# Performance work log

Measured on AMD Instinct MI355X. Metric: run time of the kernel, lower is better.

Reference implementation:

```python
import jax, jax.numpy as jnp
import numpy as np

N = 8192
IN_DIM = 256
HID = 512
NUM_CLASSES = 256
AVG_DEG = 32


def setup_inputs() -> dict:
    key = jax.random.key(0)
    k_a, k_x, k_w1, k_w2 = jax.random.split(key, 4)
    # Binary adjacency with avg degree ~AVG_DEG (entries are exactly 1.0, matching
    # A.nonzero() edge extraction with implicit unit edge weights).
    A = (jax.random.uniform(k_a, (N, N)) < (AVG_DEG / N)).astype(jnp.float32)
    x = jax.random.normal(k_x, (N, IN_DIM), dtype=jnp.float32)
    # GCNConv params: glorot-ish weights, zero bias.
    W1 = jax.random.normal(k_w1, (IN_DIM, HID), dtype=jnp.float32) / np.sqrt(IN_DIM)
    b1 = jnp.zeros((HID,), dtype=jnp.float32)
    W2 = jax.random.normal(k_w2, (HID, NUM_CLASSES), dtype=jnp.float32) / np.sqrt(HID)
    b2 = jnp.zeros((NUM_CLASSES,), dtype=jnp.float32)
    sigmoid_param = jnp.array([10.0], dtype=jnp.float32)
    return {"A": A, "x": x, "W1": W1, "b1": b1, "W2": W2, "b2": b2,
            "sigmoid_param": sigmoid_param}


def _gcn_propagate(A, deg_inv_sqrt, h):
    # PyG GCNConv aggregation with self-loops, without materializing A + I:
    # out_j = d_j^{-1/2} * sum_i A_ij d_i^{-1/2} h_i  +  d_j^{-1} h_j
    m = deg_inv_sqrt[:, None] * h              # [N, d]
    agg = A.T @ m                              # messages flow row -> col
    return deg_inv_sqrt[:, None] * agg + (deg_inv_sqrt[:, None] ** 2) * h


def reference(A, x, W1, b1, W2, b2, sigmoid_param):
    # Degree from column sums of (A + I) — matches gcn_norm's scatter on col.
    deg = jnp.sum(A, axis=0) + 1.0             # [N], >= 1 thanks to self-loop
    deg_inv_sqrt = jax.lax.rsqrt(deg)
    skip_x = x                                  # nn.Identity skip connection
    # GCNConv 1: linear then normalized aggregation, then bias; ReLU.
    h = _gcn_propagate(A, deg_inv_sqrt, x @ W1) + b1
    h = jax.nn.relu(h)
    # GCNConv 2.
    h = _gcn_propagate(A, deg_inv_sqrt, h @ W2) + b2
    # Skip add + scaled sigmoid (original casts to double; kept float32 here).
    return jax.nn.sigmoid(sigmoid_param * (h + skip_x))
```

## Files before the change

kernel.cpp:

```cpp
#include <hip/hip_runtime.h>
#include <hip/hip_bf16.h>

#define N_NODES 8192
#define IN_DIM  256
#define HID     512
#define NCLS    256
#define CAP     128

typedef __attribute__((ext_vector_type(8))) __bf16 bf16x8;
typedef __attribute__((ext_vector_type(4))) float  floatx4;

static __device__ __forceinline__ float bf2f(ushort u) {
    union { float f; unsigned int i; } v; v.i = ((unsigned int)u) << 16; return v.f;
}
static __device__ __forceinline__ ushort f2bf(float f) {
    __hip_bfloat16 b = __float2bfloat16(f);
    return *reinterpret_cast<ushort*>(&b);
}
static __device__ __forceinline__ void bfpair(unsigned int u, float& lo, float& hi) {
    union { float f; unsigned int i; } a, b;
    a.i = u << 16; b.i = u & 0xFFFF0000u;
    lo = a.f; hi = b.f;
}

__global__ __launch_bounds__(256) void build_csc(const float* __restrict__ A,
                                                 int* __restrict__ col_cnt,
                                                 int* __restrict__ col_idx) {
    const int jbase = (blockIdx.x * 256 + threadIdx.x) * 4;
    const int i0 = blockIdx.y * 32;
    for (int ii = 0; ii < 32; ++ii) {
        const int i = i0 + ii;
        const floatx4* p = reinterpret_cast<const floatx4*>(A + (size_t)i * N_NODES + jbase);
        floatx4 v = __builtin_nontemporal_load(p);
        if (v.x != 0.0f) { int q = atomicAdd(&col_cnt[jbase + 0], 1); if (q < CAP) col_idx[(size_t)(jbase + 0) * CAP + q] = i; }
        if (v.y != 0.0f) { int q = atomicAdd(&col_cnt[jbase + 1], 1); if (q < CAP) col_idx[(size_t)(jbase + 1) * CAP + q] = i; }
        if (v.z != 0.0f) { int q = atomicAdd(&col_cnt[jbase + 2], 1); if (q < CAP) col_idx[(size_t)(jbase + 2) * CAP + q] = i; }
        if (v.w != 0.0f) { int q = atomicAdd(&col_cnt[jbase + 3], 1); if (q < CAP) col_idx[(size_t)(jbase + 3) * CAP + q] = i; }
    }
}

__global__ __launch_bounds__(256) void prep_misc(const float* __restrict__ x,
                                                 const float* __restrict__ W1,
                                                 const float* __restrict__ W2,
                                                 const int* __restrict__ col_cnt,
                                                 ushort* __restrict__ xb,
                                                 float* __restrict__ dis,
                                                 ushort* __restrict__ W1Th, ushort* __restrict__ W1Tl,
                                                 ushort* __restrict__ W2Th, ushort* __restrict__ W2Tl) {
    const int idx = blockIdx.x * 256 + threadIdx.x;
    {
        const int i = idx * 4;
        const floatx4 v = *reinterpret_cast<const floatx4*>(x + i);
        *reinterpret_cast<ushort4*>(xb + i) = ushort4{f2bf(v.x), f2bf(v.y), f2bf(v.z), f2bf(v.w)};
    }
    if (idx < N_NODES)
        dis[idx] = rsqrtf((float)col_cnt[idx] + 1.0f);
    if (idx < IN_DIM * HID) {
        {
            const int k = idx / HID, n = idx % HID;
            const float v = W1[idx]; const ushort h = f2bf(v);
            W1Th[(size_t)n * IN_DIM + k] = h;
            W1Tl[(size_t)n * IN_DIM + k] = f2bf(v - bf2f(h));
        }
        {
            const int k = idx / NCLS, n = idx % NCLS;
            const float v = W2[idx]; const ushort h = f2bf(v);
            W2Th[(size_t)n * HID + k] = h;
            W2Tl[(size_t)n * HID + k] = f2bf(v - bf2f(h));
        }
    }
}

__global__ __launch_bounds__(256) void agg_x(const ushort* __restrict__ xb,
                                             const int* __restrict__ col_idx,
                                             const int* __restrict__ col_cnt,
                                             const float* __restrict__ dis,
                                             ushort* __restrict__ px) {
    const int j = __builtin_amdgcn_readfirstlane(blockIdx.x * 4 + (threadIdx.x >> 6));
    const int d = (threadIdx.x & 63) * 4;
    const int cnt = min(col_cnt[j], CAP);
    const float dj = dis[j];
    float a0, a1, a2, a3;
    {
        const uint2 sv = *reinterpret_cast<const uint2*>(xb + (size_t)j * IN_DIM + d);
        float f0, f1, f2, f3;
        bfpair(sv.x, f0, f1); bfpair(sv.y, f2, f3);
        a0 = dj * f0; a1 = dj * f1; a2 = dj * f2; a3 = dj * f3;
    }
    const int* __restrict__ lst = col_idx + (size_t)j * CAP;
    int e = 0;
    for (; e + 8 <= cnt; e += 8) {
        uint2 rv[8]; float we[8];
#pragma unroll
        for (int q = 0; q < 8; ++q) {
            const int i = lst[e + q];
            rv[q] = *reinterpret_cast<const uint2*>(xb + (size_t)i * IN_DIM + d);
            we[q] = dis[i];
        }
#pragma unroll
        for (int q = 0; q < 8; ++q) {
            float f0, f1, f2, f3;
            bfpair(rv[q].x, f0, f1); bfpair(rv[q].y, f2, f3);
            a0 += we[q] * f0; a1 += we[q] * f1; a2 += we[q] * f2; a3 += we[q] * f3;
        }
    }
    for (; e < cnt; ++e) {
        const int i = lst[e];
        const uint2 rv = *reinterpret_cast<const uint2*>(xb + (size_t)i * IN_DIM + d);
        const float we = dis[i];
        float f0, f1, f2, f3;
        bfpair(rv.x, f0, f1); bfpair(rv.y, f2, f3);
        a0 += we * f0; a1 += we * f1; a2 += we * f2; a3 += we * f3;
    }
    a0 *= dj; a1 *= dj; a2 *= dj; a3 *= dj;
    *reinterpret_cast<ushort4*>(px + (size_t)j * IN_DIM + d) =
        ushort4{f2bf(a0), f2bf(a1), f2bf(a2), f2bf(a3)};
}

template<int K>
__device__ __forceinline__ void gemm_core44(const ushort* __restrict__ A,
                                            const ushort* __restrict__ Bh,
                                            const ushort* __restrict__ Bl,
                                            int m_base, int n_base,
                                            int l16, int quad, floatx4 acc[4][4]) {
#pragma unroll 2
    for (int k0 = 0; k0 < K; k0 += 32) {
        const int kf = k0 + quad * 8;
        bf16x8 a[4], bh[4], bl[4];
#pragma unroll
        for (int t = 0; t < 4; ++t)
            a[t] = *reinterpret_cast<const bf16x8*>(A + (size_t)(m_base + t * 16 + l16) * K + kf);
#pragma unroll
        for (int t = 0; t < 4; ++t) {
            const size_t bo = (size_t)(n_base + t * 16 + l16) * K + kf;
            bh[t] = *reinterpret_cast<const bf16x8*>(Bh + bo);
            bl[t] = *reinterpret_cast<const bf16x8*>(Bl + bo);
        }
#pragma unroll
        for (int tm = 0; tm < 4; ++tm)
#pragma unroll
            for (int tn = 0; tn < 4; ++tn) {
                acc[tm][tn] = __builtin_amdgcn_mfma_f32_16x16x32_bf16(a[tm], bl[tn], acc[tm][tn], 0, 0, 0);
                acc[tm][tn] = __builtin_amdgcn_mfma_f32_16x16x32_bf16(a[tm], bh[tn], acc[tm][tn], 0, 0, 0);
            }
    }
}

template<int K>
__device__ __forceinline__ void gemm_core42(const ushort* __restrict__ A,
                                            const ushort* __restrict__ Bh,
                                            const ushort* __restrict__ Bl,
                                            int m_base, int n_base,
                                            int l16, int quad, floatx4 acc[4][2]) {
#pragma unroll 2
    for (int k0 = 0; k0 < K; k0 += 32) {
        const int kf = k0 + quad * 8;
        bf16x8 a[4], bh[2], bl[2];
#pragma unroll
        for (int t = 0; t < 4; ++t)
            a[t] = *reinterpret_cast<const bf16x8*>(A + (size_t)(m_base + t * 16 + l16) * K + kf);
#pragma unroll
        for (int t = 0; t < 2; ++t) {
            const size_t bo = (size_t)(n_base + t * 16 + l16) * K + kf;
            bh[t] = *reinterpret_cast<const bf16x8*>(Bh + bo);
            bl[t] = *reinterpret_cast<const bf16x8*>(Bl + bo);
        }
#pragma unroll
        for (int tm = 0; tm < 4; ++tm)
#pragma unroll
            for (int tn = 0; tn < 2; ++tn) {
                acc[tm][tn] = __builtin_amdgcn_mfma_f32_16x16x32_bf16(a[tm], bl[tn], acc[tm][tn], 0, 0, 0);
                acc[tm][tn] = __builtin_amdgcn_mfma_f32_16x16x32_bf16(a[tm], bh[tn], acc[tm][tn], 0, 0, 0);
            }
    }
}

__global__ __launch_bounds__(256) void gemm1_fused(const ushort* __restrict__ A,
                                                   const ushort* __restrict__ Bh,
                                                   const ushort* __restrict__ Bl,
                                                   const float* __restrict__ b1,
                                                   ushort* __restrict__ h) {
    const int tid = threadIdx.x;
    const int lane = tid & 63, wave = tid >> 6;
    const int wm = wave >> 1, wn = wave & 1;
    const int l16 = lane & 15, quad = lane >> 4;
    const int m_base = blockIdx.x * 128 + wm * 64;
    const int n_base = blockIdx.y * 128 + wn * 64;
    floatx4 acc[4][4] = {};
    gemm_core44<IN_DIM>(A, Bh, Bl, m_base, n_base, l16, quad, acc);
#pragma unroll
    for (int tn = 0; tn < 4; ++tn) {
        const int col = n_base + tn * 16 + l16;
        const float bv = b1[col];
#pragma unroll
        for (int tm = 0; tm < 4; ++tm)
#pragma unroll
            for (int r = 0; r < 4; ++r) {
                const int row = m_base + tm * 16 + quad * 4 + r;
                h[(size_t)row * HID + col] = f2bf(fmaxf(acc[tm][tn][r] + bv, 0.0f));
            }
    }
}

__global__ __launch_bounds__(256) void gemm2(const ushort* __restrict__ A,
                                             const ushort* __restrict__ Bh,
                                             const ushort* __restrict__ Bl,
                                             ushort* __restrict__ g2b) {
    const int tid = threadIdx.x;
    const int lane = tid & 63, wave = tid >> 6;
    const int wm = wave >> 1, wn = wave & 1;
    const int l16 = lane & 15, quad = lane >> 4;
    const int m_base = blockIdx.x * 128 + wm * 64;
    const int n_base = blockIdx.y * 64 + wn * 32;
    floatx4 acc[4][2] = {};
    gemm_core42<HID>(A, Bh, Bl, m_base, n_base, l16, quad, acc);
#pragma unroll
    for (int tm = 0; tm < 4; ++tm)
#pragma unroll
        for (int tn = 0; tn < 2; ++tn)
#pragma unroll
            for (int r = 0; r < 4; ++r)
                g2b[(size_t)(m_base + tm * 16 + quad * 4 + r) * NCLS + (n_base + tn * 16 + l16)] =
                    f2bf(acc[tm][tn][r]);
}

__global__ __launch_bounds__(256) void agg_out(const ushort* __restrict__ g2b,
                                               const int* __restrict__ col_idx,
                                               const int* __restrict__ col_cnt,
                                               const float* __restrict__ dis,
                                               const float* __restrict__ b2,
                                               const float* __restrict__ x,
                                               const float* __restrict__ sp_p,
                                               float* __restrict__ out) {
    const int j = __builtin_amdgcn_readfirstlane(blockIdx.x * 4 + (threadIdx.x >> 6));
    const int d = (threadIdx.x & 63) * 4;
    const int cnt = min(col_cnt[j], CAP);
    const float dj = dis[j];
    float a0, a1, a2, a3;
    {
        const uint2 sv = *reinterpret_cast<const uint2*>(g2b + (size_t)j * NCLS + d);
        float f0, f1, f2, f3;
        bfpair(sv.x, f0, f1); bfpair(sv.y, f2, f3);
        a0 = dj * f0; a1 = dj * f1; a2 = dj * f2; a3 = dj * f3;
    }
    const int* __restrict__ lst = col_idx + (size_t)j * CAP;
    int e = 0;
    for (; e + 8 <= cnt; e += 8) {
        uint2 rv[8]; float we[8];
#pragma unroll
        for (int q = 0; q < 8; ++q) {
            const int i = lst[e + q];
            rv[q] = *reinterpret_cast<const uint2*>(g2b + (size_t)i * NCLS + d);
            we[q] = dis[i];
        }
#pragma unroll
        for (int q = 0; q < 8; ++q) {
            float f0, f1, f2, f3;
            bfpair(rv[q].x, f0, f1); bfpair(rv[q].y, f2, f3);
            a0 += we[q] * f0; a1 += we[q] * f1; a2 += we[q] * f2; a3 += we[q] * f3;
        }
    }
    for (; e < cnt; ++e) {
        const int i = lst[e];
        const uint2 rv = *reinterpret_cast<const uint2*>(g2b + (size_t)i * NCLS + d);
        const float we = dis[i];
        float f0, f1, f2, f3;
        bfpair(rv.x, f0, f1); bfpair(rv.y, f2, f3);
        a0 += we * f0; a1 += we * f1; a2 += we * f2; a3 += we * f3;
    }
    const float sp = sp_p[0];
    const floatx4 bv = *reinterpret_cast<const floatx4*>(b2 + d);
    const floatx4 xv = __builtin_nontemporal_load(
        reinterpret_cast<const floatx4*>(x + (size_t)j * NCLS + d));
    floatx4 o;
    o.x = 1.0f / (1.0f + __expf(-sp * (dj * a0 + bv.x + xv.x)));
    o.y = 1.0f / (1.0f + __expf(-sp * (dj * a1 + bv.y + xv.y)));
    o.z = 1.0f / (1.0f + __expf(-sp * (dj * a2 + bv.z + xv.z)));
    o.w = 1.0f / (1.0f + __expf(-sp * (dj * a3 + bv.w + xv.w)));
    __builtin_nontemporal_store(o, reinterpret_cast<floatx4*>(out + (size_t)j * NCLS + d));
}

extern "C" void kernel_launch(void* const* d_in, const int* in_sizes, int n_in,
                              void* d_out, int out_size, void* d_ws, size_t ws_size,
                              hipStream_t stream) {
    const float* A  = (const float*)d_in[0];
    const float* x  = (const float*)d_in[1];
    const float* W1 = (const float*)d_in[2];
    const float* b1 = (const float*)d_in[3];
    const float* W2 = (const float*)d_in[4];
    const float* b2 = (const float*)d_in[5];
    const float* sp = (const float*)d_in[6];
    float* out = (float*)d_out;

    char* ws = (char*)d_ws;
    size_t off = 0;
    auto alloc = [&](size_t bytes) {
        void* p = ws + off;
        off = (off + bytes + 255) & ~(size_t)255;
        return p;
    };
    int*    col_cnt = (int*)   alloc((size_t)N_NODES * 4);
    float*  dis     = (float*) alloc((size_t)N_NODES * 4);
    int*    col_idx = (int*)   alloc((size_t)N_NODES * CAP * 4);
    ushort* xb      = (ushort*)alloc((size_t)N_NODES * IN_DIM * 2);
    ushort* px      = (ushort*)alloc((size_t)N_NODES * IN_DIM * 2);
    ushort* W1Th    = (ushort*)alloc((size_t)HID * IN_DIM * 2);
    ushort* W1Tl    = (ushort*)alloc((size_t)HID * IN_DIM * 2);
    ushort* W2Th    = (ushort*)alloc((size_t)NCLS * HID * 2);
    ushort* W2Tl    = (ushort*)alloc((size_t)NCLS * HID * 2);
    ushort* h       = (ushort*)alloc((size_t)N_NODES * HID * 2);
    ushort* g2b     = (ushort*)alloc((size_t)N_NODES * NCLS * 2);

    (void)hipMemsetAsync(col_cnt, 0, (size_t)N_NODES * 4, stream);

    build_csc<<<dim3(8, 256), 256, 0, stream>>>(A, col_cnt, col_idx);
    prep_misc<<<(N_NODES * IN_DIM / 4) / 256, 256, 0, stream>>>(
        x, W1, W2, col_cnt, xb, dis, W1Th, W1Tl, W2Th, W2Tl);

    agg_x<<<N_NODES / 4, 256, 0, stream>>>(xb, col_idx, col_cnt, dis, px);
    gemm1_fused<<<dim3(N_NODES / 128, HID / 128), 256, 0, stream>>>(
        px, W1Th, W1Tl, b1, h);

    gemm2<<<dim3(N_NODES / 128, NCLS / 64), 256, 0, stream>>>(
        h, W2Th, W2Tl, g2b);
    agg_out<<<N_NODES / 4, 256, 0, stream>>>(g2b, col_idx, col_cnt, dis, b2, x, sp, out);
}
```

Baseline: 427.8 us.

## Fuse both GEMMs into one kernel keeping hidden activations in LDS

Merges the first GEMM (with bias and ReLU) and the second GEMM into a single kernel. Each block computes a 32-row slab of the hidden layer across all 512 columns into shared memory, then multiplies it by W2 directly from LDS. This removes the global write and re-read of the 8192x512 hidden tensor and one kernel launch. In exchange, each block now reloads the full W1 and W2 hi/lo weights for only 32 rows, and there are fewer, larger blocks holding 16 accumulator tiles per wave, which raises register pressure and may lower occupancy.

```diff
diff --git a/kernel.cpp b/kernel.cpp
--- a/kernel.cpp
+++ b/kernel.cpp
@@ -6,6 +6,7 @@
 #define HID     512
 #define NCLS    256
 #define CAP     128
+#define LDSK    (HID + 8)
 
 typedef __attribute__((ext_vector_type(8))) __bf16 bf16x8;
 typedef __attribute__((ext_vector_type(4))) float  floatx4;
@@ -117,111 +118,91 @@
         ushort4{f2bf(a0), f2bf(a1), f2bf(a2), f2bf(a3)};
 }
 
-template<int K>
-__device__ __forceinline__ void gemm_core44(const ushort* __restrict__ A,
-                                            const ushort* __restrict__ Bh,
-                                            const ushort* __restrict__ Bl,
-                                            int m_base, int n_base,
-                                            int l16, int quad, floatx4 acc[4][4]) {
-#pragma unroll 2
-    for (int k0 = 0; k0 < K; k0 += 32) {
-        const int kf = k0 + quad * 8;
-        bf16x8 a[4], bh[4], bl[4];
-#pragma unroll
-        for (int t = 0; t < 4; ++t)
-            a[t] = *reinterpret_cast<const bf16x8*>(A + (size_t)(m_base + t * 16 + l16) * K + kf);
-#pragma unroll
-        for (int t = 0; t < 4; ++t) {
-            const size_t bo = (size_t)(n_base + t * 16 + l16) * K + kf;
-            bh[t] = *reinterpret_cast<const bf16x8*>(Bh + bo);
-            bl[t] = *reinterpret_cast<const bf16x8*>(Bl + bo);
-        }
-#pragma unroll
-        for (int tm = 0; tm < 4; ++tm)
-#pragma unroll
-            for (int tn = 0; tn < 4; ++tn) {
-                acc[tm][tn] = __builtin_amdgcn_mfma_f32_16x16x32_bf16(a[tm], bl[tn], acc[tm][tn], 0, 0, 0);
-                acc[tm][tn] = __builtin_amdgcn_mfma_f32_16x16x32_bf16(a[tm], bh[tn], acc[tm][tn], 0, 0, 0);
-            }
-    }
-}
-
-template<int K>
-__device__ __forceinline__ void gemm_core42(const ushort* __restrict__ A,
-                                            const ushort* __restrict__ Bh,
-                                            const ushort* __restrict__ Bl,
-                                            int m_base, int n_base,
-                                            int l16, int quad, floatx4 acc[4][2]) {
-#pragma unroll 2
-    for (int k0 = 0; k0 < K; k0 += 32) {
-        const int kf = k0 + quad * 8;
-        bf16x8 a[4], bh[2], bl[2];
-#pragma unroll
-        for (int t = 0; t < 4; ++t)
-            a[t] = *reinterpret_cast<const bf16x8*>(A + (size_t)(m_base + t * 16 + l16) * K + kf);
-#pragma unroll
-        for (int t = 0; t < 2; ++t) {
-            const size_t bo = (size_t)(n_base + t * 16 + l16) * K + kf;
-            bh[t] = *reinterpret_cast<const bf16x8*>(Bh + bo);
-            bl[t] = *reinterpret_cast<const bf16x8*>(Bl + bo);
-        }
-#pragma unroll
-        for (int tm = 0; tm < 4; ++tm)
-#pragma unroll
-            for (int tn = 0; tn < 2; ++tn) {
-                acc[tm][tn] = __builtin_amdgcn_mfma_f32_16x16x32_bf16(a[tm], bl[tn], acc[tm][tn], 0, 0, 0);
-                acc[tm][tn] = __builtin_amdgcn_mfma_f32_16x16x32_bf16(a[tm], bh[tn], acc[tm][tn], 0, 0, 0);
-            }
-    }
-}
-
-__global__ __launch_bounds__(256) void gemm1_fused(const ushort* __restrict__ A,
-                                                   const ushort* __restrict__ Bh,
-                                                   const ushort* __restrict__ Bl,
-                                                   const float* __restrict__ b1,
-                                                   ushort* __restrict__ h) {
+__global__ __launch_bounds__(256) void gemm12_fused(const ushort* __restrict__ A,
+                                                    const ushort* __restrict__ B1h,
+                                                    const ushort* __restrict__ B1l,
+                                                    const float* __restrict__ b1,
+                                                    const ushort* __restrict__ B2h,
+                                                    const ushort* __restrict__ B2l,
+                                                    ushort* __restrict__ g2b) {
+    __shared__ ushort hs[32 * LDSK];
     const int tid = threadIdx.x;
     const int lane = tid & 63, wave = tid >> 6;
-    const int wm = wave >> 1, wn = wave & 1;
     const int l16 = lane & 15, quad = lane >> 4;
-    const int m_base = blockIdx.x * 128 + wm * 64;
-    const int n_base = blockIdx.y * 128 + wn * 64;
-    floatx4 acc[4][4] = {};
-    gemm_core44<IN_DIM>(A, Bh, Bl, m_base, n_base, l16, quad, acc);
-#pragma unroll
-    for (int tn = 0; tn < 4; ++tn) {
-        const int col = n_base + tn * 16 + l16;
-        const float bv = b1[col];
-#pragma unroll
-        for (int tm = 0; tm < 4; ++tm)
-#pragma unroll
-            for (int r = 0; r < 4; ++r) {
-                const int row = m_base + tm * 16 + quad * 4 + r;
-                h[(size_t)row * HID + col] = f2bf(fmaxf(acc[tm][tn][r] + bv, 0.0f));
+    const int m_blk = blockIdx.x * 32;
+
+    {
+        const int n_base = wave * 128;
+        floatx4 acc[2][8] = {};
+#pragma unroll 1
+        for (int k0 = 0; k0 < IN_DIM; k0 += 32) {
+            const int kf = k0 + quad * 8;
+            bf16x8 a[2], bh[8], bl[8];
+#pragma unroll
+            for (int t = 0; t < 2; ++t)
+                a[t] = *reinterpret_cast<const bf16x8*>(A + (size_t)(m_blk + t * 16 + l16) * IN_DIM + kf);
+#pragma unroll
+            for (int t = 0; t < 8; ++t) {
+                const size_t bo = (size_t)(n_base + t * 16 + l16) * IN_DIM + kf;
+                bh[t] = *reinterpret_cast<const bf16x8*>(B1h + bo);
+                bl[t] = *reinterpret_cast<const bf16x8*>(B1l + bo);
             }
-    }
-}
-
-__global__ __launch_bounds__(256) void gemm2(const ushort* __restrict__ A,
-                                             const ushort* __restrict__ Bh,
-                                             const ushort* __restrict__ Bl,
-                                             ushort* __restrict__ g2b) {
-    const int tid = threadIdx.x;
-    const int lane = tid & 63, wave = tid >> 6;
-    const int wm = wave >> 1, wn = wave & 1;
-    const int l16 = lane & 15, quad = lane >> 4;
-    const int m_base = blockIdx.x * 128 + wm * 64;
-    const int n_base = blockIdx.y * 64 + wn * 32;
-    floatx4 acc[4][2] = {};
-    gemm_core42<HID>(A, Bh, Bl, m_base, n_base, l16, quad, acc);
-#pragma unroll
-    for (int tm = 0; tm < 4; ++tm)
-#pragma unroll
-        for (int tn = 0; tn < 2; ++tn)
-#pragma unroll
-            for (int r = 0; r < 4; ++r)
-                g2b[(size_t)(m_base + tm * 16 + quad * 4 + r) * NCLS + (n_base + tn * 16 + l16)] =
-                    f2bf(acc[tm][tn][r]);
+#pragma unroll
+            for (int tm = 0; tm < 2; ++tm)
+#pragma unroll
+                for (int tn = 0; tn < 8; ++tn) {
+                    acc[tm][tn] = __builtin_amdgcn_mfma_f32_16x16x32_bf16(a[tm], bl[tn], acc[tm][tn], 0, 0, 0);
+                    acc[tm][tn] = __builtin_amdgcn_mfma_f32_16x16x32_bf16(a[tm], bh[tn], acc[tm][tn], 0, 0, 0);
+                }
+        }
+#pragma unroll
+        for (int tn = 0; tn < 8; ++tn) {
+            const int col = n_base + tn * 16 + l16;
+            const float bv = b1[col];
+#pragma unroll
+            for (int tm = 0; tm < 2; ++tm)
+#pragma unroll
+                for (int r = 0; r < 4; ++r) {
+                    const int row = tm * 16 + quad * 4 + r;
+                    hs[row * LDSK + col] = f2bf(fmaxf(acc[tm][tn][r] + bv, 0.0f));
+                }
+        }
+    }
+    __syncthreads();
+
+    {
+        const int n_base = wave * 64;
+        floatx4 acc[2][4] = {};
+#pragma unroll 2
+        for (int k0 = 0; k0 < HID; k0 += 32) {
+            const int kf = k0 + quad * 8;
+            bf16x8 a[2], bh[4], bl[4];
+#pragma unroll
+            for (int t = 0; t < 2; ++t)
+                a[t] = *reinterpret_cast<const bf16x8*>(hs + (size_t)(t * 16 + l16) * LDSK + kf);
+#pragma unroll
+            for (int t = 0; t < 4; ++t) {
+                const size_t bo = (size_t)(n_base + t * 16 + l16) * HID + kf;
+                bh[t] = *reinterpret_cast<const bf16x8*>(B2h + bo);
+                bl[t] = *reinterpret_cast<const bf16x8*>(B2l + bo);
+            }
+#pragma unroll
+            for (int tm = 0; tm < 2; ++tm)
+#pragma unroll
+                for (int tn = 0; tn < 4; ++tn) {
+                    acc[tm][tn] = __builtin_amdgcn_mfma_f32_16x16x32_bf16(a[tm], bl[tn], acc[tm][tn], 0, 0, 0);
+                    acc[tm][tn] = __builtin_amdgcn_mfma_f32_16x16x32_bf16(a[tm], bh[tn], acc[tm][tn], 0, 0, 0);
+                }
+        }
+#pragma unroll
+        for (int tm = 0; tm < 2; ++tm)
+#pragma unroll
+            for (int tn = 0; tn < 4; ++tn)
+#pragma unroll
+                for (int r = 0; r < 4; ++r)
+                    g2b[(size_t)(m_blk + tm * 16 + quad * 4 + r) * NCLS + (n_base + tn * 16 + l16)] =
+                        f2bf(acc[tm][tn][r]);
+    }
 }
 
 __global__ __launch_bounds__(256) void agg_out(const ushort* __restrict__ g2b,
@@ -308,7 +289,6 @@
     ushort* W1Tl    = (ushort*)alloc((size_t)HID * IN_DIM * 2);
     ushort* W2Th    = (ushort*)alloc((size_t)NCLS * HID * 2);
     ushort* W2Tl    = (ushort*)alloc((size_t)NCLS * HID * 2);
-    ushort* h       = (ushort*)alloc((size_t)N_NODES * HID * 2);
     ushort* g2b     = (ushort*)alloc((size_t)N_NODES * NCLS * 2);
 
     (void)hipMemsetAsync(col_cnt, 0, (size_t)N_NODES * 4, stream);
@@ -318,10 +298,8 @@
         x, W1, W2, col_cnt, xb, dis, W1Th, W1Tl, W2Th, W2Tl);
 
     agg_x<<<N_NODES / 4, 256, 0, stream>>>(xb, col_idx, col_cnt, dis, px);
-    gemm1_fused<<<dim3(N_NODES / 128, HID / 128), 256, 0, stream>>>(
-        px, W1Th, W1Tl, b1, h);
-
-    gemm2<<<dim3(N_NODES / 128, NCLS / 64), 256, 0, stream>>>(
-        h, W2Th, W2Tl, g2b);
+    gemm12_fused<<<N_NODES / 32, 256, 0, stream>>>(
+        px, W1Th, W1Tl, b1, W2Th, W2Tl, g2b);
+
     agg_out<<<N_NODES / 4, 256, 0, stream>>>(g2b, col_idx, col_cnt, dis, b2, x, sp, out);
 }
```

New measurement: 430.0 us. About the same (+0.5%).
